# Performance work log

Hardware: AMD Instinct MI355X
Metric: run time of the kernel (lower is better)

The kernel has to match this reference:

```python
import jax, jax.numpy as jnp
import numpy as np

SQRT2 = float(np.sqrt(2.0))

# near_sym_b biort filters (13,19)-tap, as used by DTCWT level 1
_H0O = np.array([-0.0017578, 0.0, 0.0222656, -0.046875, -0.0482422, 0.296875,
                 0.5554688, 0.296875, -0.0482422, -0.046875, 0.0222656, 0.0,
                 -0.0017578], np.float32)
_H1O = np.array([-0.0000706, 0.0, 0.0013419, -0.0018834, -0.0071568, 0.023856,
                 0.0556431, -0.0516881, -0.2997576, 0.5594308, -0.2997576,
                 -0.0516881, 0.0556431, 0.023856, -0.0071568, -0.0018834,
                 0.0013419, 0.0, -0.0000706], np.float32)

def _sgn(L):
    return np.where((np.arange(L) - L // 2) % 2 == 0, 1.0, -1.0).astype(np.float32)

# synthesis filters: G0(z)=H1(-z), G1(z)=-H0(-z) (zero-phase centered)
_G0O = _H1O * _sgn(19)
_G1O = -(_H0O * _sgn(13))


def _filt(x, h, axis):
    # separable symmetric-extension FIR filter along H (axis=2) or W (axis=3)
    L = int(h.shape[0]); m = L // 2
    pad = [(0, 0)] * 4
    pad[axis] = (m, m)
    xp = jnp.pad(x, pad, mode='symmetric')
    k = h.reshape((1, 1, L, 1)) if axis == 2 else h.reshape((1, 1, 1, L))
    B, C = x.shape[0], x.shape[1]
    y = jax.lax.conv_general_dilated(
        xp.reshape((B * C, 1) + xp.shape[2:]), k,
        window_strides=(1, 1), padding='VALID',
        dimension_numbers=('NCHW', 'OIHW', 'NCHW'))
    return y.reshape(x.shape)


def _q2c(y):
    # quad pixels -> two complex subimages
    y = y * (1.0 / SQRT2)
    a = y[..., 0::2, 0::2]; b = y[..., 0::2, 1::2]
    c = y[..., 1::2, 0::2]; d = y[..., 1::2, 1::2]
    return (a - d, b + c), (a + d, b - c)


def _c2q(w1r, w1i, w2r, w2i):
    B, C, H2, W2 = w1r.shape
    top = jnp.stack([w1r + w2r, w1i + w2i], axis=-1).reshape(B, C, H2, 2 * W2)
    bot = jnp.stack([w1i - w2i, w2r - w1r], axis=-1).reshape(B, C, H2, 2 * W2)
    return jnp.stack([top, bot], axis=-2).reshape(B, C, 2 * H2, 2 * W2) * (1.0 / SQRT2)


def _dtcwt_fwd(x, h0, h1):
    lo = _filt(x, h0, 3); hi = _filt(x, h1, 3)
    ll = _filt(lo, h0, 2)
    lh = _filt(lo, h1, 2); hl = _filt(hi, h0, 2); hh = _filt(hi, h1, 2)
    lhp, lhq = _q2c(lh); hlp, hlq = _q2c(hl); hhp, hhq = _q2c(hh)
    bands = [lhp, hhp, hlp, hlq, hhq, lhq]  # 15,45,75,105,135,165 degrees
    reals = jnp.stack([b[0] for b in bands], axis=2)
    imags = jnp.stack([b[1] for b in bands], axis=2)
    return ll, jnp.stack([reals, imags], axis=-1)  # (B,C,H,W), (B,C,6,H/2,W/2,2)


def _dtcwt_inv(ll, yh, g0, g1):
    r, im = yh[..., 0], yh[..., 1]
    lh = _c2q(r[:, :, 0], im[:, :, 0], r[:, :, 5], im[:, :, 5])
    hl = _c2q(r[:, :, 2], im[:, :, 2], r[:, :, 3], im[:, :, 3])
    hh = _c2q(r[:, :, 1], im[:, :, 1], r[:, :, 4], im[:, :, 4])
    lo = _filt(ll, g0, 2) + _filt(lh, g1, 2)
    hi = _filt(hl, g0, 2) + _filt(hh, g1, 2)
    return _filt(lo, g0, 3) + _filt(hi, g1, 3)


def _dwconv(x, w, b):
    y = jax.lax.conv_general_dilated(
        x, w, window_strides=(1, 1), padding='SAME',
        feature_group_count=w.shape[0],
        dimension_numbers=('NCHW', 'OIHW', 'NCHW'))
    return y + b[None, :, None, None]


def _forward(x, conv_w, conv_b, w_ll, w_lh1, w_lh2, b_lh1, b_lh2,
             w_t1, w_t2, b_t1, b_t2, H, W):
    B, N, C = x.shape
    Ch = C // 2
    xi_ = x.reshape(B, H, W, C).transpose(0, 3, 1, 2)  # (B,C,H,W)
    x1, x2 = xi_[:, :Ch], xi_[:, Ch:]
    x1 = _dwconv(x1, conv_w, conv_b)
    h0 = jnp.asarray(_H0O); h1 = jnp.asarray(_H1O)
    xl, xh = _dtcwt_fwd(x2, h0, h1)
    xl = xl * w_ll
    H2, W2 = H // 2, W // 2
    nb = 4; bs = Ch // nb
    mul = lambda t, w: jnp.einsum('...bd,bdk->...bk', t, w)
    # channel mixing: block-diagonal complex MLP over channel blocks
    xp = jnp.transpose(xh, (5, 0, 2, 3, 4, 1)).reshape(2, B, 6, H2, W2, nb, bs)
    xr, xim = xp[0], xp[1]
    xr1 = jax.nn.relu(mul(xr, w_lh1[0]) - mul(xim, w_lh1[1]) + b_lh1[0])
    xi1 = jax.nn.relu(mul(xr, w_lh1[1]) + mul(xim, w_lh1[0]) + b_lh1[1])
    xr2 = mul(xr1, w_lh2[0]) - mul(xi1, w_lh2[1]) + b_lh2[0]
    xi2 = mul(xr1, w_lh2[1]) + mul(xi1, w_lh2[0]) + b_lh2[1]
    cm = jnp.stack([xr2, xi2], -1).reshape(B, 6, H2, W2, Ch, 2)
    t = jnp.transpose(cm, (5, 0, 4, 1, 2, 3))  # (2,B,Ch,6,H2,W2)
    tr, ti = t[0], t[1]
    tr1 = jax.nn.relu(mul(tr, w_t1[0]) - mul(ti, w_t1[1]) + b_t1[0])
    ti1 = jax.nn.relu(mul(tr, w_t1[1]) + mul(ti, w_t1[0]) + b_t1[1])
    tr2 = mul(tr1, w_t2[0]) - mul(ti1, w_t2[1]) + b_t2[0]
    ti2 = mul(tr1, w_t2[1]) + mul(ti1, w_t2[0]) + b_t2[1]
    yh = jnp.stack([tr2, ti2], -1)  # (B,Ch,6,H2,W2,2)
    x2r = _dtcwt_inv(xl, yh, jnp.asarray(_G0O), jnp.asarray(_G1O))
    out = jnp.concatenate([x1, x2r], axis=1)
    return out.transpose(0, 2, 3, 1).reshape(B, N, C)


def setup_inputs() -> dict:
    key = jax.random.key(0)
    ks = jax.random.split(key, 12)
    B, H, W, C = 256, 28, 28, 128
    Ch = C // 2
    nb, bs, tb = 4, Ch // 4, 14
    return {
        'x': jax.random.normal(ks[0], (B, H * W, C), jnp.float32),
        'conv_w': jax.random.normal(ks[1], (Ch, 1, 3, 3), jnp.float32) * 0.1,
        'conv_b': jnp.zeros((Ch,), jnp.float32),
        'w_ll': jax.random.normal(ks[2], (Ch, H, W), jnp.float32) * 0.02,
        'w_lh1': jax.random.normal(ks[3], (2, nb, bs, bs), jnp.float32) * 0.02,
        'w_lh2': jax.random.normal(ks[4], (2, nb, bs, bs), jnp.float32) * 0.02,
        'b_lh1': jax.random.normal(ks[5], (2, nb, bs), jnp.float32) * 0.02,
        'b_lh2': jax.random.normal(ks[6], (2, nb, bs), jnp.float32) * 0.02,
        'w_t1': jax.random.normal(ks[7], (2, tb, tb, tb), jnp.float32) * 0.02,
        'w_t2': jax.random.normal(ks[8], (2, tb, tb, tb), jnp.float32) * 0.02,
        'b_t1': jax.random.normal(ks[9], (2, tb, tb), jnp.float32) * 0.02,
        'b_t2': jax.random.normal(ks[10], (2, tb, tb), jnp.float32) * 0.02,
        'H': H, 'W': W,
    }


def reference(x, conv_w, conv_b, w_ll, w_lh1, w_lh2, b_lh1, b_lh2,
              w_t1, w_t2, b_t1, b_t2, H, W):
    return _forward(x, conv_w, conv_b, w_ll, w_lh1, w_lh2, b_lh1, b_lh2,
                    w_t1, w_t2, b_t1, b_t2, H, W)
```

## Files before the change

kernel.cpp:

```cpp
#include <hip/hip_runtime.h>


#define DI __device__ __forceinline__

__device__ constexpr float F_H0[13] = {
  -0.0017578f, 0.0f, 0.0222656f, -0.046875f, -0.0482422f, 0.296875f,
   0.5554688f, 0.296875f, -0.0482422f, -0.046875f, 0.0222656f, 0.0f, -0.0017578f};
__device__ constexpr float F_H1[19] = {
  -7.06e-05f, 0.0f, 0.0013419f, -0.0018834f, -0.0071568f, 0.023856f,
   0.0556431f, -0.0516881f, -0.2997576f, 0.5594308f, -0.2997576f, -0.0516881f,
   0.0556431f, 0.023856f, -0.0071568f, -0.0018834f, 0.0013419f, 0.0f, -7.06e-05f};
__device__ constexpr float F_G0[19] = {
   7.06e-05f, 0.0f, -0.0013419f, -0.0018834f, 0.0071568f, 0.023856f,
  -0.0556431f, -0.0516881f, 0.2997576f, 0.5594308f, 0.2997576f, -0.0516881f,
  -0.0556431f, 0.023856f, 0.0071568f, -0.0018834f, -0.0013419f, 0.0f, 7.06e-05f};
__device__ constexpr float F_G1[13] = {
   0.0017578f, 0.0f, -0.0222656f, -0.046875f, 0.0482422f, 0.296875f,
  -0.5554688f, 0.296875f, 0.0482422f, -0.046875f, -0.0222656f, 0.0f, 0.0017578f};

DI constexpr int refl28(int i) { return i < 0 ? -1 - i : (i >= 28 ? 55 - i : i); }

#define S2C 0.70710678118654752f

__global__ __launch_bounds__(256) void k_dwconv(const float* __restrict__ x,
    const float* __restrict__ cw, const float* __restrict__ cb,
    float* __restrict__ out) {
  int tid = blockIdx.x * 256 + threadIdx.x;
  int c = tid & 63;
  int s = tid >> 6;
  int w = s % 28; int t2 = s / 28; int h = t2 % 28;
  const float* k = cw + c * 9;
  const float* xb = x + (size_t)s * 128 + c;
  float acc = cb[c];
  bool hm = h > 0, hp = h < 27, wm = w > 0, wp = w < 27;
  if (hm) {
    const float* r = xb - 28 * 128;
    if (wm) acc = fmaf(r[-128], k[0], acc);
    acc = fmaf(r[0], k[1], acc);
    if (wp) acc = fmaf(r[128], k[2], acc);
  }
  if (wm) acc = fmaf(xb[-128], k[3], acc);
  acc = fmaf(xb[0], k[4], acc);
  if (wp) acc = fmaf(xb[128], k[5], acc);
  if (hp) {
    const float* r = xb + 28 * 128;
    if (wm) acc = fmaf(r[-128], k[6], acc);
    acc = fmaf(r[0], k[7], acc);
    if (wp) acc = fmaf(r[128], k[8], acc);
  }
  out[(size_t)s * 128 + c] = acc;
}

__global__ __launch_bounds__(256) void k_rowfilt(const float* __restrict__ x,
    float* __restrict__ lo, float* __restrict__ hi) {
  int tid = threadIdx.x;
  int c = tid & 63;
  int line = blockIdx.x * 4 + (tid >> 6);
  const float* xp = x + (size_t)line * 28 * 128 + 64 + c;
  float v[28];
#pragma unroll
  for (int w = 0; w < 28; w++) v[w] = xp[w * 128];
  float* lp = lo + (size_t)line * 28 * 64 + c;
  float* hp = hi + (size_t)line * 28 * 64 + c;
#pragma unroll
  for (int w = 0; w < 28; w++) {
    float aLo = 0.f, aHi = 0.f;
#pragma unroll
    for (int t = 0; t < 13; t++) aLo = fmaf(F_H0[t], v[refl28(w - 6 + t)], aLo);
#pragma unroll
    for (int t = 0; t < 19; t++) aHi = fmaf(F_H1[t], v[refl28(w - 9 + t)], aHi);
    lp[w * 64] = aLo;
    hp[w * 64] = aHi;
  }
}

__global__ __launch_bounds__(256) void k_colfilt(const float* __restrict__ lo,
    const float* __restrict__ hi, const float* __restrict__ wll,
    float* __restrict__ xl, float* __restrict__ xhr, float* __restrict__ xhi) {
  __shared__ float swll[3584];
  int tid = threadIdx.x;
  int w2 = blockIdx.x >> 6;
  for (int j = tid; j < 3584; j += 256) {
    int cc = j & 63, t = j >> 6;
    int h = t >> 1, woff = t & 1;
    swll[j] = wll[cc * 784 + h * 28 + 2 * w2 + woff];
  }
  __syncthreads();
  int c = tid & 63;
  int unit = blockIdx.x * 4 + (tid >> 6);
  int b = unit & 255;
  const int hs = 28 * 64;
  int base_in = (b * 784 + 2 * w2) * 64 + c;
  float v0[28], v1[28];
#pragma unroll
  for (int h = 0; h < 28; h++) {
    v0[h] = lo[base_in + h * hs];
    v1[h] = lo[base_in + h * hs + 64];
  }
#pragma unroll
  for (int h = 0; h < 28; h++) {
    float a0 = 0.f, a1 = 0.f;
#pragma unroll
    for (int t = 0; t < 13; t++) {
      a0 = fmaf(F_H0[t], v0[refl28(h - 6 + t)], a0);
      a1 = fmaf(F_H0[t], v1[refl28(h - 6 + t)], a1);
    }
    int o = (b * 784 + h * 28 + 2 * w2) * 64 + c;
    xl[o]      = a0 * swll[(h * 2 + 0) * 64 + c];
    xl[o + 64] = a1 * swll[(h * 2 + 1) * 64 + c];
  }
  {
    float e0[28], e1[28];
#pragma unroll
    for (int h = 0; h < 28; h++) {
      float a0 = 0.f, a1 = 0.f;
#pragma unroll
      for (int t = 0; t < 19; t++) {
        a0 = fmaf(F_H1[t], v0[refl28(h - 9 + t)], a0);
        a1 = fmaf(F_H1[t], v1[refl28(h - 9 + t)], a1);
      }
      e0[h] = a0; e1[h] = a1;
    }
    int bb = (b * 6 * 196 + w2) * 64 + c;
#pragma unroll
    for (int i = 0; i < 14; i++) {
      float A = e0[2 * i], Bv = e1[2 * i], C = e0[2 * i + 1], D = e1[2 * i + 1];
      xhr[bb + 0 * 12544 + i * 896] = (A - D) * S2C;
      xhi[bb + 0 * 12544 + i * 896] = (Bv + C) * S2C;
      xhr[bb + 5 * 12544 + i * 896] = (A + D) * S2C;
      xhi[bb + 5 * 12544 + i * 896] = (Bv - C) * S2C;
    }
  }
#pragma unroll
  for (int h = 0; h < 28; h++) {
    v0[h] = hi[base_in + h * hs];
    v1[h] = hi[base_in + h * hs + 64];
  }
  {
    float e0[28], e1[28];
#pragma unroll
    for (int h = 0; h < 28; h++) {
      float a0 = 0.f, a1 = 0.f;
#pragma unroll
      for (int t = 0; t < 13; t++) {
        a0 = fmaf(F_H0[t], v0[refl28(h - 6 + t)], a0);
        a1 = fmaf(F_H0[t], v1[refl28(h - 6 + t)], a1);
      }
      e0[h] = a0; e1[h] = a1;
    }
    int bb = (b * 6 * 196 + w2) * 64 + c;
#pragma unroll
    for (int i = 0; i < 14; i++) {
      float A = e0[2 * i], Bv = e1[2 * i], C = e0[2 * i + 1], D = e1[2 * i + 1];
      xhr[bb + 2 * 12544 + i * 896] = (A - D) * S2C;
      xhi[bb + 2 * 12544 + i * 896] = (Bv + C) * S2C;
      xhr[bb + 3 * 12544 + i * 896] = (A + D) * S2C;
      xhi[bb + 3 * 12544 + i * 896] = (Bv - C) * S2C;
    }
  }
  {
    float e0[28], e1[28];
#pragma unroll
    for (int h = 0; h < 28; h++) {
      float a0 = 0.f, a1 = 0.f;
#pragma unroll
      for (int t = 0; t < 19; t++) {
        a0 = fmaf(F_H1[t], v0[refl28(h - 9 + t)], a0);
        a1 = fmaf(F_H1[t], v1[refl28(h - 9 + t)], a1);
      }
      e0[h] = a0; e1[h] = a1;
    }
    int bb = (b * 6 * 196 + w2) * 64 + c;
#pragma unroll
    for (int i = 0; i < 14; i++) {
      float A = e0[2 * i], Bv = e1[2 * i], C = e0[2 * i + 1], D = e1[2 * i + 1];
      xhr[bb + 1 * 12544 + i * 896] = (A - D) * S2C;
      xhi[bb + 1 * 12544 + i * 896] = (Bv + C) * S2C;
      xhr[bb + 4 * 12544 + i * 896] = (A + D) * S2C;
      xhi[bb + 4 * 12544 + i * 896] = (Bv - C) * S2C;
    }
  }
}

__global__ __launch_bounds__(256) void k_chmix(float* __restrict__ xhr,
    float* __restrict__ xhi,
    const float* __restrict__ w1, const float* __restrict__ w2,
    const float* __restrict__ b1, const float* __restrict__ b2) {
  __shared__ __align__(16) float sw1[2048];
  __shared__ __align__(16) float sw2[2048];
  __shared__ __align__(16) float sb1[128];
  __shared__ __align__(16) float sb2[128];
  int tid = threadIdx.x;
  for (int i = tid; i < 1024; i += 256) {
    int dk = i >> 2, blk = i & 3;
    int li = dk * 8 + blk * 2;
    sw1[li]     = w1[blk * 256 + dk];
    sw1[li + 1] = w1[1024 + blk * 256 + dk];
    sw2[li]     = w2[blk * 256 + dk];
    sw2[li + 1] = w2[1024 + blk * 256 + dk];
  }
  if (tid < 64) {
    int k = tid >> 2, blk = tid & 3;
    int li = k * 8 + blk * 2;
    sb1[li] = b1[blk * 16 + k]; sb1[li + 1] = b1[64 + blk * 16 + k];
    sb2[li] = b2[blk * 16 + k]; sb2[li + 1] = b2[64 + blk * 16 + k];
  }
  __syncthreads();
  int idx = blockIdx.x * 256 + tid;
  int blk = idx & 3;
  int p = idx >> 2;
  size_t base = (size_t)p * 64 + blk * 16;
  float xr[16], xi[16];
  const float4* pr = (const float4*)(xhr + base);
  const float4* pi = (const float4*)(xhi + base);
#pragma unroll
  for (int j = 0; j < 4; j++) {
    float4 a = pr[j];
    xr[4 * j] = a.x; xr[4 * j + 1] = a.y; xr[4 * j + 2] = a.z; xr[4 * j + 3] = a.w;
    float4 bb = pi[j];
    xi[4 * j] = bb.x; xi[4 * j + 1] = bb.y; xi[4 * j + 2] = bb.z; xi[4 * j + 3] = bb.w;
  }
  int wb = blk * 2;
  float yr[16], yi[16];
#pragma unroll
  for (int k = 0; k < 16; k++) {
    float2 bv = *(const float2*)(sb1 + k * 8 + wb);
    float ar = bv.x, ai = bv.y;
#pragma unroll
    for (int d = 0; d < 16; d++) {
      float2 wv = *(const float2*)(sw1 + (d * 16 + k) * 8 + wb);
      ar = fmaf(xr[d], wv.x, ar); ar = fmaf(-xi[d], wv.y, ar);
      ai = fmaf(xr[d], wv.y, ai); ai = fmaf(xi[d], wv.x, ai);
    }
    yr[k] = fmaxf(ar, 0.f); yi[k] = fmaxf(ai, 0.f);
  }
#pragma unroll
  for (int k = 0; k < 16; k++) {
    float2 bv = *(const float2*)(sb2 + k * 8 + wb);
    float ar = bv.x, ai = bv.y;
#pragma unroll
    for (int d = 0; d < 16; d++) {
      float2 wv = *(const float2*)(sw2 + (d * 16 + k) * 8 + wb);
      ar = fmaf(yr[d], wv.x, ar); ar = fmaf(-yi[d], wv.y, ar);
      ai = fmaf(yr[d], wv.y, ai); ai = fmaf(yi[d], wv.x, ai);
    }
    xr[k] = ar; xi[k] = ai;
  }
  float4* qr = (float4*)(xhr + base);
  float4* qi = (float4*)(xhi + base);
#pragma unroll
  for (int j = 0; j < 4; j++) {
    qr[j] = make_float4(xr[4 * j], xr[4 * j + 1], xr[4 * j + 2], xr[4 * j + 3]);
    qi[j] = make_float4(xi[4 * j], xi[4 * j + 1], xi[4 * j + 2], xi[4 * j + 3]);
  }
}

__global__ __launch_bounds__(256) void k_tokmix(float* __restrict__ xhr,
    float* __restrict__ xhi,
    const float* __restrict__ wt1, const float* __restrict__ wt2,
    const float* __restrict__ bt1, const float* __restrict__ bt2) {
  __shared__ __align__(16) float st1[5488];
  __shared__ __align__(16) float st2[5488];
  __shared__ __align__(16) float sB1[392];
  __shared__ __align__(16) float sB2[392];
  int tid = threadIdx.x;
  for (int i = tid; i < 2744; i += 256) {
    st1[2 * i] = wt1[i]; st1[2 * i + 1] = wt1[2744 + i];
    st2[2 * i] = wt2[i]; st2[2 * i + 1] = wt2[2744 + i];
  }
  for (int i = tid; i < 196; i += 256) {
    sB1[2 * i] = bt1[i]; sB1[2 * i + 1] = bt1[196 + i];
    sB2[2 * i] = bt2[i]; sB2[2 * i + 1] = bt2[196 + i];
  }
  __syncthreads();
  int idx = blockIdx.x * 256 + tid;
  int c = idx & 63;
  int pp = idx >> 6;
  int h2 = pp % 14;
  int baseA = pp * 896 + c;
  int baseB = (pp + 10752) * 896 + c;
  float trA[14], tiA[14], trB[14], tiB[14];
#pragma unroll
  for (int d = 0; d < 14; d++) {
    trA[d] = xhr[baseA + d * 64]; tiA[d] = xhi[baseA + d * 64];
    trB[d] = xhr[baseB + d * 64]; tiB[d] = xhi[baseB + d * 64];
  }
  const float* w1 = st1 + h2 * 392;
  const float* w2 = st2 + h2 * 392;
  const float* bb1 = sB1 + h2 * 28;
  const float* bb2 = sB2 + h2 * 28;
  float mrA[14], miA[14], mrB[14], miB[14];
#pragma unroll
  for (int k = 0; k < 14; k++) {
    float br = bb1[2 * k], bi = bb1[2 * k + 1];
    float arA = br, aiA = bi, arB = br, aiB = bi;
#pragma unroll
    for (int d = 0; d < 14; d++) {
      float wr = w1[(d * 14 + k) * 2], wi = w1[(d * 14 + k) * 2 + 1];
      arA = fmaf(trA[d], wr, arA); arA = fmaf(-tiA[d], wi, arA);
      aiA = fmaf(trA[d], wi, aiA); aiA = fmaf(tiA[d], wr, aiA);
      arB = fmaf(trB[d], wr, arB); arB = fmaf(-tiB[d], wi, arB);
      aiB = fmaf(trB[d], wi, aiB); aiB = fmaf(tiB[d], wr, aiB);
    }
    mrA[k] = fmaxf(arA, 0.f); miA[k] = fmaxf(aiA, 0.f);
    mrB[k] = fmaxf(arB, 0.f); miB[k] = fmaxf(aiB, 0.f);
  }
#pragma unroll
  for (int k = 0; k < 14; k++) {
    float br = bb2[2 * k], bi = bb2[2 * k + 1];
    float arA = br, aiA = bi, arB = br, aiB = bi;
#pragma unroll
    for (int d = 0; d < 14; d++) {
      float wr = w2[(d * 14 + k) * 2], wi = w2[(d * 14 + k) * 2 + 1];
      arA = fmaf(mrA[d], wr, arA); arA = fmaf(-miA[d], wi, arA);
      aiA = fmaf(mrA[d], wi, aiA); aiA = fmaf(miA[d], wr, aiA);
      arB = fmaf(mrB[d], wr, arB); arB = fmaf(-miB[d], wi, arB);
      aiB = fmaf(mrB[d], wi, aiB); aiB = fmaf(miB[d], wr, aiB);
    }
    xhr[baseA + k * 64] = arA; xhi[baseA + k * 64] = aiA;
    xhr[baseB + k * 64] = arB; xhi[baseB + k * 64] = aiB;
  }
}

__global__ __launch_bounds__(256) void k_invcol(const float* __restrict__ xl,
    const float* __restrict__ xhr, const float* __restrict__ xhi,
    float* __restrict__ lo2, float* __restrict__ hi2) {
  int tid = threadIdx.x;
  int c = tid & 63;
  int line = blockIdx.x * 4 + (tid >> 6);
  int w = line % 28, b = line / 28;
  int w2 = w >> 1, pw = w & 1;
  const int hs = 28 * 64;
  int sp = (b * 784 + w) * 64 + c;
  int bb = (b * 6 * 196 + w2) * 64 + c;
  {
    float xlv[28], lhf[28];
#pragma unroll
    for (int h = 0; h < 28; h++) xlv[h] = xl[sp + h * hs];
    const float* p0r = xhr + bb + 0 * 12544;
    const float* p0i = xhi + bb + 0 * 12544;
    const float* p5r = xhr + bb + 5 * 12544;
    const float* p5i = xhi + bb + 5 * 12544;
#pragma unroll
    for (int i = 0; i < 14; i++) {
      float y0r = p0r[i * 896], y0i = p0i[i * 896];
      float y5r = p5r[i * 896], y5i = p5i[i * 896];
      float top, bot;
      if (pw) { top = y0i + y5i; bot = y5r - y0r; }
      else    { top = y0r + y5r; bot = y0i - y5i; }
      lhf[2 * i] = top * S2C; lhf[2 * i + 1] = bot * S2C;
    }
#pragma unroll
    for (int h = 0; h < 28; h++) {
      float acc = 0.f;
#pragma unroll
      for (int t = 0; t < 19; t++) acc = fmaf(F_G0[t], xlv[refl28(h - 9 + t)], acc);
#pragma unroll
      for (int t = 0; t < 13; t++) acc = fmaf(F_G1[t], lhf[refl28(h - 6 + t)], acc);
      lo2[sp + h * hs] = acc;
    }
  }
  {
    float hlC[28], hhD[28];
    const float* p2r = xhr + bb + 2 * 12544;
    const float* p2i = xhi + bb + 2 * 12544;
    const float* p3r = xhr + bb + 3 * 12544;
    const float* p3i = xhi + bb + 3 * 12544;
#pragma unroll
    for (int i = 0; i < 14; i++) {
      float y0r = p2r[i * 896], y0i = p2i[i * 896];
      float y5r = p3r[i * 896], y5i = p3i[i * 896];
      float top, bot;
      if (pw) { top = y0i + y5i; bot = y5r - y0r; }
      else    { top = y0r + y5r; bot = y0i - y5i; }
      hlC[2 * i] = top * S2C; hlC[2 * i + 1] = bot * S2C;
    }
    const float* p1r = xhr + bb + 1 * 12544;
    const float* p1i = xhi + bb + 1 * 12544;
    const float* p4r = xhr + bb + 4 * 12544;
    const float* p4i = xhi + bb + 4 * 12544;
#pragma unroll
    for (int i = 0; i < 14; i++) {
      float y0r = p1r[i * 896], y0i = p1i[i * 896];
      float y5r = p4r[i * 896], y5i = p4i[i * 896];
      float top, bot;
      if (pw) { top = y0i + y5i; bot = y5r - y0r; }
      else    { top = y0r + y5r; bot = y0i - y5i; }
      hhD[2 * i] = top * S2C; hhD[2 * i + 1] = bot * S2C;
    }
#pragma unroll
    for (int h = 0; h < 28; h++) {
      float acc = 0.f;
#pragma unroll
      for (int t = 0; t < 19; t++) acc = fmaf(F_G0[t], hlC[refl28(h - 9 + t)], acc);
#pragma unroll
      for (int t = 0; t < 13; t++) acc = fmaf(F_G1[t], hhD[refl28(h - 6 + t)], acc);
      hi2[sp + h * hs] = acc;
    }
  }
}

__global__ __launch_bounds__(256) void k_invrow(const float* __restrict__ lo2,
    const float* __restrict__ hi2, float* __restrict__ out) {
  int tid = threadIdx.x;
  int c = tid & 63;
  int line = blockIdx.x * 4 + (tid >> 6);
  const float* lr = lo2 + (size_t)line * 28 * 64 + c;
  const float* hr = hi2 + (size_t)line * 28 * 64 + c;
  float vl[28], vh[28];
#pragma unroll
  for (int w = 0; w < 28; w++) { vl[w] = lr[w * 64]; vh[w] = hr[w * 64]; }
  float* op = out + (size_t)line * 28 * 128 + 64 + c;
#pragma unroll
  for (int w = 0; w < 28; w++) {
    float acc = 0.f;
#pragma unroll
    for (int t = 0; t < 19; t++) acc = fmaf(F_G0[t], vl[refl28(w - 9 + t)], acc);
#pragma unroll
    for (int t = 0; t < 13; t++) acc = fmaf(F_G1[t], vh[refl28(w - 6 + t)], acc);
    op[w * 128] = acc;
  }
}

extern "C" void kernel_launch(void* const* d_in, const int* in_sizes, int n_in,
                              void* d_out, int out_size, void* d_ws, size_t ws_size,
                              hipStream_t stream) {
  const float* x    = (const float*)d_in[0];
  const float* cw   = (const float*)d_in[1];
  const float* cb   = (const float*)d_in[2];
  const float* wll  = (const float*)d_in[3];
  const float* wlh1 = (const float*)d_in[4];
  const float* wlh2 = (const float*)d_in[5];
  const float* blh1 = (const float*)d_in[6];
  const float* blh2 = (const float*)d_in[7];
  const float* wt1  = (const float*)d_in[8];
  const float* wt2  = (const float*)d_in[9];
  const float* bt1  = (const float*)d_in[10];
  const float* bt2  = (const float*)d_in[11];
  float* out = (float*)d_out;
  float* ws = (float*)d_ws;

  const size_t NSP = (size_t)256 * 784 * 64;
  const size_t NXH = (size_t)256 * 6 * 196 * 64;
  float* lo  = ws;
  float* hi  = lo + NSP;
  float* xl  = hi + NSP;
  float* xhr = xl + NSP;
  float* xhi = xhr + NXH;

  dim3 blk(256);
  k_dwconv <<<50176, blk, 0, stream>>>(x, cw, cb, out);
  k_rowfilt<<<1792,  blk, 0, stream>>>(x, lo, hi);
  k_colfilt<<<896,   blk, 0, stream>>>(lo, hi, wll, xl, xhr, xhi);
  k_chmix  <<<4704,  blk, 0, stream>>>(xhr, xhi, wlh1, wlh2, blh1, blh2);
  k_tokmix <<<2688,  blk, 0, stream>>>(xhr, xhi, wt1, wt2, bt1, bt2);
  k_invcol <<<1792,  blk, 0, stream>>>(xl, xhr, xhi, lo, hi);
  k_invrow <<<1792,  blk, 0, stream>>>(lo, hi, out);
  (void)in_sizes; (void)n_in; (void)out_size; (void)ws_size;
}
```

Baseline: 694.4 us.

## Fuse forward and inverse row/column DTCWT filters through LDS tiles; restage channel mix

Merges the forward row and column filter passes into one kernel that holds per-image, 8-channel row-filtered tiles in shared memory. It does the same for the inverse column and row passes, which removes the lo/hi intermediate round trips through global memory and cuts two launches. The channel-mix kernel now stages its tile through padded LDS with float4 global accesses, reads weights straight from global/scalar memory, and computes each output row in a register-blocked loop. The trade-offs are heavy register and LDS use per block, idle threads in the 224-of-256 mapping, and narrower 8-channel groups that may reduce global access coalescing.

```diff
diff --git a/kernel.cpp b/kernel.cpp
--- a/kernel.cpp
+++ b/kernel.cpp
@@ -21,6 +21,8 @@
 DI constexpr int refl28(int i) { return i < 0 ? -1 - i : (i >= 28 ? 55 - i : i); }
 
 #define S2C 0.70710678118654752f
+#define LH(h, w, c) ((h) * 285 + (w) * 10 + (c))
+#define LDS_TILE 7980
 
 __global__ __launch_bounds__(256) void k_dwconv(const float* __restrict__ x,
     const float* __restrict__ cw, const float* __restrict__ cb,
@@ -51,134 +53,125 @@
   out[(size_t)s * 128 + c] = acc;
 }
 
-__global__ __launch_bounds__(256) void k_rowfilt(const float* __restrict__ x,
-    float* __restrict__ lo, float* __restrict__ hi) {
-  int tid = threadIdx.x;
-  int c = tid & 63;
-  int line = blockIdx.x * 4 + (tid >> 6);
-  const float* xp = x + (size_t)line * 28 * 128 + 64 + c;
-  float v[28];
-#pragma unroll
-  for (int w = 0; w < 28; w++) v[w] = xp[w * 128];
-  float* lp = lo + (size_t)line * 28 * 64 + c;
-  float* hp = hi + (size_t)line * 28 * 64 + c;
-#pragma unroll
-  for (int w = 0; w < 28; w++) {
-    float aLo = 0.f, aHi = 0.f;
-#pragma unroll
-    for (int t = 0; t < 13; t++) aLo = fmaf(F_H0[t], v[refl28(w - 6 + t)], aLo);
-#pragma unroll
-    for (int t = 0; t < 19; t++) aHi = fmaf(F_H1[t], v[refl28(w - 9 + t)], aHi);
-    lp[w * 64] = aLo;
-    hp[w * 64] = aHi;
-  }
-}
-
-__global__ __launch_bounds__(256) void k_colfilt(const float* __restrict__ lo,
-    const float* __restrict__ hi, const float* __restrict__ wll,
+DI void write_bands(float* __restrict__ xhr, float* __restrict__ xhi,
+    int b, int bp, int bq, int S, int w2, int c64,
+    const float* e0, const float* e1) {
+#pragma unroll
+  for (int ii = 0; ii < 7; ii++) {
+    int i = 7 * S + ii;
+    float A = e0[2 * ii], Bv = e1[2 * ii], C = e0[2 * ii + 1], D = e1[2 * ii + 1];
+    int op = ((b * 6 + bp) * 196 + i * 14 + w2) * 64 + c64;
+    int oq = ((b * 6 + bq) * 196 + i * 14 + w2) * 64 + c64;
+    xhr[op] = (A - D) * S2C; xhi[op] = (Bv + C) * S2C;
+    xhr[oq] = (A + D) * S2C; xhi[oq] = (Bv - C) * S2C;
+  }
+}
+
+template <int S>
+DI void fwd_phase2(const float* __restrict__ sL, const float* __restrict__ sH,
+    int b, int cg, int w2, int c, const float* __restrict__ wll,
     float* __restrict__ xl, float* __restrict__ xhr, float* __restrict__ xhi) {
-  __shared__ float swll[3584];
-  int tid = threadIdx.x;
-  int w2 = blockIdx.x >> 6;
-  for (int j = tid; j < 3584; j += 256) {
-    int cc = j & 63, t = j >> 6;
-    int h = t >> 1, woff = t & 1;
-    swll[j] = wll[cc * 784 + h * 28 + 2 * w2 + woff];
-  }
-  __syncthreads();
-  int c = tid & 63;
-  int unit = blockIdx.x * 4 + (tid >> 6);
-  int b = unit & 255;
-  const int hs = 28 * 64;
-  int base_in = (b * 784 + 2 * w2) * 64 + c;
+  int c64 = cg * 8 + c;
   float v0[28], v1[28];
 #pragma unroll
   for (int h = 0; h < 28; h++) {
-    v0[h] = lo[base_in + h * hs];
-    v1[h] = lo[base_in + h * hs + 64];
-  }
+    v0[h] = sL[LH(h, 2 * w2, c)];
+    v1[h] = sL[LH(h, 2 * w2 + 1, c)];
+  }
+#pragma unroll
+  for (int j = 0; j < 14; j++) {
+    int h = 14 * S + j;
+    float a0 = 0.f, a1 = 0.f;
+#pragma unroll
+    for (int t = 0; t < 13; t++) {
+      int idx = refl28(14 * S + j - 6 + t);
+      a0 = fmaf(F_H0[t], v0[idx], a0);
+      a1 = fmaf(F_H0[t], v1[idx], a1);
+    }
+    int o = (b * 784 + h * 28 + 2 * w2) * 64 + c64;
+    xl[o]      = a0 * wll[c64 * 784 + h * 28 + 2 * w2];
+    xl[o + 64] = a1 * wll[c64 * 784 + h * 28 + 2 * w2 + 1];
+  }
+  float e0[14], e1[14];
+#pragma unroll
+  for (int j = 0; j < 14; j++) {
+    float a0 = 0.f, a1 = 0.f;
+#pragma unroll
+    for (int t = 0; t < 19; t++) {
+      int idx = refl28(14 * S + j - 9 + t);
+      a0 = fmaf(F_H1[t], v0[idx], a0);
+      a1 = fmaf(F_H1[t], v1[idx], a1);
+    }
+    e0[j] = a0; e1[j] = a1;
+  }
+  write_bands(xhr, xhi, b, 0, 5, S, w2, c64, e0, e1);
 #pragma unroll
   for (int h = 0; h < 28; h++) {
+    v0[h] = sH[LH(h, 2 * w2, c)];
+    v1[h] = sH[LH(h, 2 * w2 + 1, c)];
+  }
+#pragma unroll
+  for (int j = 0; j < 14; j++) {
     float a0 = 0.f, a1 = 0.f;
 #pragma unroll
     for (int t = 0; t < 13; t++) {
-      a0 = fmaf(F_H0[t], v0[refl28(h - 6 + t)], a0);
-      a1 = fmaf(F_H0[t], v1[refl28(h - 6 + t)], a1);
-    }
-    int o = (b * 784 + h * 28 + 2 * w2) * 64 + c;
-    xl[o]      = a0 * swll[(h * 2 + 0) * 64 + c];
-    xl[o + 64] = a1 * swll[(h * 2 + 1) * 64 + c];
-  }
-  {
-    float e0[28], e1[28];
-#pragma unroll
-    for (int h = 0; h < 28; h++) {
-      float a0 = 0.f, a1 = 0.f;
-#pragma unroll
-      for (int t = 0; t < 19; t++) {
-        a0 = fmaf(F_H1[t], v0[refl28(h - 9 + t)], a0);
-        a1 = fmaf(F_H1[t], v1[refl28(h - 9 + t)], a1);
-      }
-      e0[h] = a0; e1[h] = a1;
-    }
-    int bb = (b * 6 * 196 + w2) * 64 + c;
-#pragma unroll
-    for (int i = 0; i < 14; i++) {
-      float A = e0[2 * i], Bv = e1[2 * i], C = e0[2 * i + 1], D = e1[2 * i + 1];
-      xhr[bb + 0 * 12544 + i * 896] = (A - D) * S2C;
-      xhi[bb + 0 * 12544 + i * 896] = (Bv + C) * S2C;
-      xhr[bb + 5 * 12544 + i * 896] = (A + D) * S2C;
-      xhi[bb + 5 * 12544 + i * 896] = (Bv - C) * S2C;
-    }
-  }
-#pragma unroll
-  for (int h = 0; h < 28; h++) {
-    v0[h] = hi[base_in + h * hs];
-    v1[h] = hi[base_in + h * hs + 64];
-  }
-  {
-    float e0[28], e1[28];
-#pragma unroll
-    for (int h = 0; h < 28; h++) {
-      float a0 = 0.f, a1 = 0.f;
-#pragma unroll
-      for (int t = 0; t < 13; t++) {
-        a0 = fmaf(F_H0[t], v0[refl28(h - 6 + t)], a0);
-        a1 = fmaf(F_H0[t], v1[refl28(h - 6 + t)], a1);
-      }
-      e0[h] = a0; e1[h] = a1;
-    }
-    int bb = (b * 6 * 196 + w2) * 64 + c;
-#pragma unroll
-    for (int i = 0; i < 14; i++) {
-      float A = e0[2 * i], Bv = e1[2 * i], C = e0[2 * i + 1], D = e1[2 * i + 1];
-      xhr[bb + 2 * 12544 + i * 896] = (A - D) * S2C;
-      xhi[bb + 2 * 12544 + i * 896] = (Bv + C) * S2C;
-      xhr[bb + 3 * 12544 + i * 896] = (A + D) * S2C;
-      xhi[bb + 3 * 12544 + i * 896] = (Bv - C) * S2C;
-    }
-  }
-  {
-    float e0[28], e1[28];
-#pragma unroll
-    for (int h = 0; h < 28; h++) {
-      float a0 = 0.f, a1 = 0.f;
-#pragma unroll
-      for (int t = 0; t < 19; t++) {
-        a0 = fmaf(F_H1[t], v0[refl28(h - 9 + t)], a0);
-        a1 = fmaf(F_H1[t], v1[refl28(h - 9 + t)], a1);
-      }
-      e0[h] = a0; e1[h] = a1;
-    }
-    int bb = (b * 6 * 196 + w2) * 64 + c;
-#pragma unroll
-    for (int i = 0; i < 14; i++) {
-      float A = e0[2 * i], Bv = e1[2 * i], C = e0[2 * i + 1], D = e1[2 * i + 1];
-      xhr[bb + 1 * 12544 + i * 896] = (A - D) * S2C;
-      xhi[bb + 1 * 12544 + i * 896] = (Bv + C) * S2C;
-      xhr[bb + 4 * 12544 + i * 896] = (A + D) * S2C;
-      xhi[bb + 4 * 12544 + i * 896] = (Bv - C) * S2C;
-    }
+      int idx = refl28(14 * S + j - 6 + t);
+      a0 = fmaf(F_H0[t], v0[idx], a0);
+      a1 = fmaf(F_H0[t], v1[idx], a1);
+    }
+    e0[j] = a0; e1[j] = a1;
+  }
+  write_bands(xhr, xhi, b, 2, 3, S, w2, c64, e0, e1);
+#pragma unroll
+  for (int j = 0; j < 14; j++) {
+    float a0 = 0.f, a1 = 0.f;
+#pragma unroll
+    for (int t = 0; t < 19; t++) {
+      int idx = refl28(14 * S + j - 9 + t);
+      a0 = fmaf(F_H1[t], v0[idx], a0);
+      a1 = fmaf(F_H1[t], v1[idx], a1);
+    }
+    e0[j] = a0; e1[j] = a1;
+  }
+  write_bands(xhr, xhi, b, 1, 4, S, w2, c64, e0, e1);
+}
+
+__global__ __launch_bounds__(256) void k_fwd(const float* __restrict__ x,
+    const float* __restrict__ wll, float* __restrict__ xl,
+    float* __restrict__ xhr, float* __restrict__ xhi) {
+  __shared__ float sL[LDS_TILE];
+  __shared__ float sH[LDS_TILE];
+  int b = blockIdx.x >> 3;
+  int cg = blockIdx.x & 7;
+  int t = threadIdx.x;
+  if (t < 224) {
+    int h = t >> 3, c = t & 7;
+    const float* xp = x + ((size_t)(b * 28 + h) * 28) * 128 + 64 + cg * 8 + c;
+    float v[28];
+#pragma unroll
+    for (int w = 0; w < 28; w++) v[w] = xp[w * 128];
+#pragma unroll
+    for (int w = 0; w < 28; w++) {
+      float a = 0.f;
+#pragma unroll
+      for (int tt = 0; tt < 13; tt++) a = fmaf(F_H0[tt], v[refl28(w - 6 + tt)], a);
+      sL[LH(h, w, c)] = a;
+    }
+#pragma unroll
+    for (int w = 0; w < 28; w++) {
+      float a = 0.f;
+#pragma unroll
+      for (int tt = 0; tt < 19; tt++) a = fmaf(F_H1[tt], v[refl28(w - 9 + tt)], a);
+      sH[LH(h, w, c)] = a;
+    }
+  }
+  __syncthreads();
+  int S = t >> 7;
+  int r = t & 127;
+  if (r < 112) {
+    int w2 = r >> 3, c = r & 7;
+    if (S == 0) fwd_phase2<0>(sL, sH, b, cg, w2, c, wll, xl, xhr, xhi);
+    else        fwd_phase2<1>(sL, sH, b, cg, w2, c, wll, xl, xhr, xhi);
   }
 }
 
@@ -186,72 +179,87 @@
     float* __restrict__ xhi,
     const float* __restrict__ w1, const float* __restrict__ w2,
     const float* __restrict__ b1, const float* __restrict__ b2) {
-  __shared__ __align__(16) float sw1[2048];
-  __shared__ __align__(16) float sw2[2048];
-  __shared__ __align__(16) float sb1[128];
-  __shared__ __align__(16) float sb2[128];
+  __shared__ float sR[64 * 66];
+  __shared__ float sI[64 * 66];
   int tid = threadIdx.x;
+  int pbase = blockIdx.x * 64;
+  const float4* gr = (const float4*)(xhr + (size_t)pbase * 64);
+  const float4* gi = (const float4*)(xhi + (size_t)pbase * 64);
+#pragma unroll
   for (int i = tid; i < 1024; i += 256) {
-    int dk = i >> 2, blk = i & 3;
-    int li = dk * 8 + blk * 2;
-    sw1[li]     = w1[blk * 256 + dk];
-    sw1[li + 1] = w1[1024 + blk * 256 + dk];
-    sw2[li]     = w2[blk * 256 + dk];
-    sw2[li + 1] = w2[1024 + blk * 256 + dk];
-  }
-  if (tid < 64) {
-    int k = tid >> 2, blk = tid & 3;
-    int li = k * 8 + blk * 2;
-    sb1[li] = b1[blk * 16 + k]; sb1[li + 1] = b1[64 + blk * 16 + k];
-    sb2[li] = b2[blk * 16 + k]; sb2[li + 1] = b2[64 + blk * 16 + k];
-  }
-  __syncthreads();
-  int idx = blockIdx.x * 256 + tid;
-  int blk = idx & 3;
-  int p = idx >> 2;
-  size_t base = (size_t)p * 64 + blk * 16;
+    int p = i >> 4, ch = (i & 15) * 4;
+    int la = p * 66 + ch;
+    float4 a = gr[i];
+    *(float2*)(sR + la)     = make_float2(a.x, a.y);
+    *(float2*)(sR + la + 2) = make_float2(a.z, a.w);
+    float4 bq = gi[i];
+    *(float2*)(sI + la)     = make_float2(bq.x, bq.y);
+    *(float2*)(sI + la + 2) = make_float2(bq.z, bq.w);
+  }
+  __syncthreads();
+  int lane = tid & 63;
+  int blk = __builtin_amdgcn_readfirstlane(tid >> 6);
+  int base = lane * 66 + blk * 16;
   float xr[16], xi[16];
-  const float4* pr = (const float4*)(xhr + base);
-  const float4* pi = (const float4*)(xhi + base);
-#pragma unroll
-  for (int j = 0; j < 4; j++) {
-    float4 a = pr[j];
-    xr[4 * j] = a.x; xr[4 * j + 1] = a.y; xr[4 * j + 2] = a.z; xr[4 * j + 3] = a.w;
-    float4 bb = pi[j];
-    xi[4 * j] = bb.x; xi[4 * j + 1] = bb.y; xi[4 * j + 2] = bb.z; xi[4 * j + 3] = bb.w;
-  }
-  int wb = blk * 2;
-  float yr[16], yi[16];
-#pragma unroll
-  for (int k = 0; k < 16; k++) {
-    float2 bv = *(const float2*)(sb1 + k * 8 + wb);
-    float ar = bv.x, ai = bv.y;
+#pragma unroll
+  for (int j = 0; j < 8; j++) {
+    float2 u = *(const float2*)(sR + base + 2 * j);
+    xr[2 * j] = u.x; xr[2 * j + 1] = u.y;
+    float2 v = *(const float2*)(sI + base + 2 * j);
+    xi[2 * j] = v.x; xi[2 * j + 1] = v.y;
+  }
+  float ar[16], ai[16];
+  {
+    const float* Wr = w1 + blk * 256;
+    const float* Wi = w1 + 1024 + blk * 256;
+#pragma unroll
+    for (int k = 0; k < 16; k++) { ar[k] = b1[blk * 16 + k]; ai[k] = b1[64 + blk * 16 + k]; }
 #pragma unroll
     for (int d = 0; d < 16; d++) {
-      float2 wv = *(const float2*)(sw1 + (d * 16 + k) * 8 + wb);
-      ar = fmaf(xr[d], wv.x, ar); ar = fmaf(-xi[d], wv.y, ar);
-      ai = fmaf(xr[d], wv.y, ai); ai = fmaf(xi[d], wv.x, ai);
-    }
-    yr[k] = fmaxf(ar, 0.f); yi[k] = fmaxf(ai, 0.f);
-  }
-#pragma unroll
-  for (int k = 0; k < 16; k++) {
-    float2 bv = *(const float2*)(sb2 + k * 8 + wb);
-    float ar = bv.x, ai = bv.y;
+      float xdr = xr[d], xdi = xi[d];
+#pragma unroll
+      for (int k = 0; k < 16; k++) {
+        float wr = Wr[d * 16 + k], wi = Wi[d * 16 + k];
+        ar[k] = fmaf(xdr, wr, ar[k]); ar[k] = fmaf(-xdi, wi, ar[k]);
+        ai[k] = fmaf(xdr, wi, ai[k]); ai[k] = fmaf( xdi, wr, ai[k]);
+      }
+    }
+#pragma unroll
+    for (int k = 0; k < 16; k++) { xr[k] = fmaxf(ar[k], 0.f); xi[k] = fmaxf(ai[k], 0.f); }
+  }
+  {
+    const float* Wr = w2 + blk * 256;
+    const float* Wi = w2 + 1024 + blk * 256;
+#pragma unroll
+    for (int k = 0; k < 16; k++) { ar[k] = b2[blk * 16 + k]; ai[k] = b2[64 + blk * 16 + k]; }
 #pragma unroll
     for (int d = 0; d < 16; d++) {
-      float2 wv = *(const float2*)(sw2 + (d * 16 + k) * 8 + wb);
-      ar = fmaf(yr[d], wv.x, ar); ar = fmaf(-yi[d], wv.y, ar);
-      ai = fmaf(yr[d], wv.y, ai); ai = fmaf(yi[d], wv.x, ai);
-    }
-    xr[k] = ar; xi[k] = ai;
-  }
-  float4* qr = (float4*)(xhr + base);
-  float4* qi = (float4*)(xhi + base);
-#pragma unroll
-  for (int j = 0; j < 4; j++) {
-    qr[j] = make_float4(xr[4 * j], xr[4 * j + 1], xr[4 * j + 2], xr[4 * j + 3]);
-    qi[j] = make_float4(xi[4 * j], xi[4 * j + 1], xi[4 * j + 2], xi[4 * j + 3]);
+      float xdr = xr[d], xdi = xi[d];
+#pragma unroll
+      for (int k = 0; k < 16; k++) {
+        float wr = Wr[d * 16 + k], wi = Wi[d * 16 + k];
+        ar[k] = fmaf(xdr, wr, ar[k]); ar[k] = fmaf(-xdi, wi, ar[k]);
+        ai[k] = fmaf(xdr, wi, ai[k]); ai[k] = fmaf( xdi, wr, ai[k]);
+      }
+    }
+  }
+  __syncthreads();
+#pragma unroll
+  for (int j = 0; j < 8; j++) {
+    *(float2*)(sR + base + 2 * j) = make_float2(ar[2 * j], ar[2 * j + 1]);
+    *(float2*)(sI + base + 2 * j) = make_float2(ai[2 * j], ai[2 * j + 1]);
+  }
+  __syncthreads();
+  float4* qr = (float4*)(xhr + (size_t)pbase * 64);
+  float4* qi = (float4*)(xhi + (size_t)pbase * 64);
+#pragma unroll
+  for (int i = tid; i < 1024; i += 256) {
+    int p = i >> 4, ch = (i & 15) * 4;
+    int la = p * 66 + ch;
+    float2 u0 = *(const float2*)(sR + la), u1 = *(const float2*)(sR + la + 2);
+    qr[i] = make_float4(u0.x, u0.y, u1.x, u1.y);
+    float2 v0 = *(const float2*)(sI + la), v1 = *(const float2*)(sI + la + 2);
+    qi[i] = make_float4(v0.x, v0.y, v1.x, v1.y);
   }
 }
 
@@ -322,103 +330,100 @@
   }
 }
 
-__global__ __launch_bounds__(256) void k_invcol(const float* __restrict__ xl,
+__global__ __launch_bounds__(256) void k_inv(const float* __restrict__ xl,
     const float* __restrict__ xhr, const float* __restrict__ xhi,
-    float* __restrict__ lo2, float* __restrict__ hi2) {
-  int tid = threadIdx.x;
-  int c = tid & 63;
-  int line = blockIdx.x * 4 + (tid >> 6);
-  int w = line % 28, b = line / 28;
-  int w2 = w >> 1, pw = w & 1;
-  const int hs = 28 * 64;
-  int sp = (b * 784 + w) * 64 + c;
-  int bb = (b * 6 * 196 + w2) * 64 + c;
-  {
-    float xlv[28], lhf[28];
-#pragma unroll
-    for (int h = 0; h < 28; h++) xlv[h] = xl[sp + h * hs];
-    const float* p0r = xhr + bb + 0 * 12544;
-    const float* p0i = xhi + bb + 0 * 12544;
-    const float* p5r = xhr + bb + 5 * 12544;
-    const float* p5i = xhi + bb + 5 * 12544;
-#pragma unroll
-    for (int i = 0; i < 14; i++) {
-      float y0r = p0r[i * 896], y0i = p0i[i * 896];
-      float y5r = p5r[i * 896], y5i = p5i[i * 896];
-      float top, bot;
-      if (pw) { top = y0i + y5i; bot = y5r - y0r; }
-      else    { top = y0r + y5r; bot = y0i - y5i; }
-      lhf[2 * i] = top * S2C; lhf[2 * i + 1] = bot * S2C;
-    }
-#pragma unroll
-    for (int h = 0; h < 28; h++) {
+    float* __restrict__ out) {
+  __shared__ float sL[LDS_TILE];
+  __shared__ float sH[LDS_TILE];
+  int b = blockIdx.x >> 3;
+  int cg = blockIdx.x & 7;
+  int t = threadIdx.x;
+  if (t < 224) {
+    int w = t >> 3, c = t & 7;
+    int c64 = cg * 8 + c;
+    int w2 = w >> 1, pw = w & 1;
+    int sp = (b * 784 + w) * 64 + c64;
+    int bb = (b * 6 * 196 + w2) * 64 + c64;
+    {
+      float xlv[28], lhf[28];
+#pragma unroll
+      for (int h = 0; h < 28; h++) xlv[h] = xl[sp + h * 1792];
+      const float* p0r = xhr + bb + 0 * 12544;
+      const float* p0i = xhi + bb + 0 * 12544;
+      const float* p5r = xhr + bb + 5 * 12544;
+      const float* p5i = xhi + bb + 5 * 12544;
+#pragma unroll
+      for (int i = 0; i < 14; i++) {
+        float y0r = p0r[i * 896], y0i = p0i[i * 896];
+        float y5r = p5r[i * 896], y5i = p5i[i * 896];
+        float top = pw ? (y0i + y5i) : (y0r + y5r);
+        float bot = pw ? (y5r - y0r) : (y0i - y5i);
+        lhf[2 * i] = top * S2C; lhf[2 * i + 1] = bot * S2C;
+      }
+#pragma unroll
+      for (int h = 0; h < 28; h++) {
+        float acc = 0.f;
+#pragma unroll
+        for (int tt = 0; tt < 19; tt++) acc = fmaf(F_G0[tt], xlv[refl28(h - 9 + tt)], acc);
+#pragma unroll
+        for (int tt = 0; tt < 13; tt++) acc = fmaf(F_G1[tt], lhf[refl28(h - 6 + tt)], acc);
+        sL[LH(h, w, c)] = acc;
+      }
+    }
+    {
+      float hlC[28], hhD[28];
+      const float* p2r = xhr + bb + 2 * 12544;
+      const float* p2i = xhi + bb + 2 * 12544;
+      const float* p3r = xhr + bb + 3 * 12544;
+      const float* p3i = xhi + bb + 3 * 12544;
+#pragma unroll
+      for (int i = 0; i < 14; i++) {
+        float y0r = p2r[i * 896], y0i = p2i[i * 896];
+        float y5r = p3r[i * 896], y5i = p3i[i * 896];
+        float top = pw ? (y0i + y5i) : (y0r + y5r);
+        float bot = pw ? (y5r - y0r) : (y0i - y5i);
+        hlC[2 * i] = top * S2C; hlC[2 * i + 1] = bot * S2C;
+      }
+      const float* p1r = xhr + bb + 1 * 12544;
+      const float* p1i = xhi + bb + 1 * 12544;
+      const float* p4r = xhr + bb + 4 * 12544;
+      const float* p4i = xhi + bb + 4 * 12544;
+#pragma unroll
+      for (int i = 0; i < 14; i++) {
+        float y0r = p1r[i * 896], y0i = p1i[i * 896];
+        float y5r = p4r[i * 896], y5i = p4i[i * 896];
+        float top = pw ? (y0i + y5i) : (y0r + y5r);
+        float bot = pw ? (y5r - y0r) : (y0i - y5i);
+        hhD[2 * i] = top * S2C; hhD[2 * i + 1] = bot * S2C;
+      }
+#pragma unroll
+      for (int h = 0; h < 28; h++) {
+        float acc = 0.f;
+#pragma unroll
+        for (int tt = 0; tt < 19; tt++) acc = fmaf(F_G0[tt], hlC[refl28(h - 9 + tt)], acc);
+#pragma unroll
+        for (int tt = 0; tt < 13; tt++) acc = fmaf(F_G1[tt], hhD[refl28(h - 6 + tt)], acc);
+        sH[LH(h, w, c)] = acc;
+      }
+    }
+  }
+  __syncthreads();
+  if (t < 224) {
+    int h = t >> 3, c = t & 7;
+    int c64 = cg * 8 + c;
+    float vl[28], vh[28];
+#pragma unroll
+    for (int w = 0; w < 28; w++) { vl[w] = sL[LH(h, w, c)]; vh[w] = sH[LH(h, w, c)]; }
+    float* op = out + ((size_t)(b * 28 + h) * 28) * 128 + 64 + c64;
+#pragma unroll
+    for (int w = 0; w < 28; w++) {
       float acc = 0.f;
 #pragma unroll
-      for (int t = 0; t < 19; t++) acc = fmaf(F_G0[t], xlv[refl28(h - 9 + t)], acc);
-#pragma unroll
-      for (int t = 0; t < 13; t++) acc = fmaf(F_G1[t], lhf[refl28(h - 6 + t)], acc);
-      lo2[sp + h * hs] = acc;
-    }
-  }
-  {
-    float hlC[28], hhD[28];
-    const float* p2r = xhr + bb + 2 * 12544;
-    const float* p2i = xhi + bb + 2 * 12544;
-    const float* p3r = xhr + bb + 3 * 12544;
-    const float* p3i = xhi + bb + 3 * 12544;
-#pragma unroll
-    for (int i = 0; i < 14; i++) {
-      float y0r = p2r[i * 896], y0i = p2i[i * 896];
-      float y5r = p3r[i * 896], y5i = p3i[i * 896];
-      float top, bot;
-      if (pw) { top = y0i + y5i; bot = y5r - y0r; }
-      else    { top = y0r + y5r; bot = y0i - y5i; }
-      hlC[2 * i] = top * S2C; hlC[2 * i + 1] = bot * S2C;
-    }
-    const float* p1r = xhr + bb + 1 * 12544;
-    const float* p1i = xhi + bb + 1 * 12544;
-    const float* p4r = xhr + bb + 4 * 12544;
-    const float* p4i = xhi + bb + 4 * 12544;
-#pragma unroll
-    for (int i = 0; i < 14; i++) {
-      float y0r = p1r[i * 896], y0i = p1i[i * 896];
-      float y5r = p4r[i * 896], y5i = p4i[i * 896];
-      float top, bot;
-      if (pw) { top = y0i + y5i; bot = y5r - y0r; }
-      else    { top = y0r + y5r; bot = y0i - y5i; }
-      hhD[2 * i] = top * S2C; hhD[2 * i + 1] = bot * S2C;
-    }
-#pragma unroll
-    for (int h = 0; h < 28; h++) {
-      float acc = 0.f;
-#pragma unroll
-      for (int t = 0; t < 19; t++) acc = fmaf(F_G0[t], hlC[refl28(h - 9 + t)], acc);
-#pragma unroll
-      for (int t = 0; t < 13; t++) acc = fmaf(F_G1[t], hhD[refl28(h - 6 + t)], acc);
-      hi2[sp + h * hs] = acc;
-    }
-  }
-}
-
-__global__ __launch_bounds__(256) void k_invrow(const float* __restrict__ lo2,
-    const float* __restrict__ hi2, float* __restrict__ out) {
-  int tid = threadIdx.x;
-  int c = tid & 63;
-  int line = blockIdx.x * 4 + (tid >> 6);
-  const float* lr = lo2 + (size_t)line * 28 * 64 + c;
-  const float* hr = hi2 + (size_t)line * 28 * 64 + c;
-  float vl[28], vh[28];
-#pragma unroll
-  for (int w = 0; w < 28; w++) { vl[w] = lr[w * 64]; vh[w] = hr[w * 64]; }
-  float* op = out + (size_t)line * 28 * 128 + 64 + c;
-#pragma unroll
-  for (int w = 0; w < 28; w++) {
-    float acc = 0.f;
-#pragma unroll
-    for (int t = 0; t < 19; t++) acc = fmaf(F_G0[t], vl[refl28(w - 9 + t)], acc);
-#pragma unroll
-    for (int t = 0; t < 13; t++) acc = fmaf(F_G1[t], vh[refl28(w - 6 + t)], acc);
-    op[w * 128] = acc;
+      for (int tt = 0; tt < 19; tt++) acc = fmaf(F_G0[tt], vl[refl28(w - 9 + tt)], acc);
+#pragma unroll
+      for (int tt = 0; tt < 13; tt++) acc = fmaf(F_G1[tt], vh[refl28(w - 6 + tt)], acc);
+      op[w * 128] = acc;
+    }
   }
 }
 
@@ -442,19 +447,15 @@
 
   const size_t NSP = (size_t)256 * 784 * 64;
   const size_t NXH = (size_t)256 * 6 * 196 * 64;
-  float* lo  = ws;
-  float* hi  = lo + NSP;
-  float* xl  = hi + NSP;
+  float* xl  = ws;
   float* xhr = xl + NSP;
   float* xhi = xhr + NXH;
 
   dim3 blk(256);
-  k_dwconv <<<50176, blk, 0, stream>>>(x, cw, cb, out);
-  k_rowfilt<<<1792,  blk, 0, stream>>>(x, lo, hi);
-  k_colfilt<<<896,   blk, 0, stream>>>(lo, hi, wll, xl, xhr, xhi);
-  k_chmix  <<<4704,  blk, 0, stream>>>(xhr, xhi, wlh1, wlh2, blh1, blh2);
-  k_tokmix <<<2688,  blk, 0, stream>>>(xhr, xhi, wt1, wt2, bt1, bt2);
-  k_invcol <<<1792,  blk, 0, stream>>>(xl, xhr, xhi, lo, hi);
-  k_invrow <<<1792,  blk, 0, stream>>>(lo, hi, out);
+  k_dwconv<<<50176, blk, 0, stream>>>(x, cw, cb, out);
+  k_fwd   <<<2048,  blk, 0, stream>>>(x, wll, xl, xhr, xhi);
+  k_chmix <<<4704,  blk, 0, stream>>>(xhr, xhi, wlh1, wlh2, blh1, blh2);
+  k_tokmix<<<2688,  blk, 0, stream>>>(xhr, xhi, wt1, wt2, bt1, bt2);
+  k_inv   <<<2048,  blk, 0, stream>>>(xl, xhr, xhi, out);
   (void)in_sizes; (void)n_in; (void)out_size; (void)ws_size;
 }
```

Measured after the change: 728.4 us. +4.9%, slower.
